# Kernel tuning notes

Hardware: AMD Instinct MI355X
Metric: run time of the kernel (lower is better)

The kernel has to match this reference:

```python
import jax, jax.numpy as jnp
import numpy as np

KNN = 4
H = 0.03


def setup_inputs() -> dict:
    key = jax.random.key(0)
    pc = jax.random.normal(key, (8, 4096, 3), dtype=jnp.float32)  # [B, N, 3]
    return {"pc": pc}


def reference(pc) -> jnp.ndarray:
    sq = jnp.sum(pc * pc, axis=-1)  # [B, N]
    # dist[b, i, j] = || pc[b,i] - pc[b,j] ||^2
    dist = sq[:, :, None] + sq[:, None, :] - 2.0 * jnp.einsum("bid,bjd->bij", pc, pc)
    dist = jnp.maximum(dist, 0.0)
    # k nearest neighbors with offset=1 (skip self): take smallest KNN+1, drop the first
    neg_top, _ = jax.lax.top_k(-dist, KNN + 1)  # sorted descending -> distances ascending
    knn_dist = -neg_top[..., 1:]  # [B, N, KNN]
    weight = jnp.exp(-knn_dist / (H * H))
    loss = jnp.sum(-knn_dist * weight)
    return loss
```

## Files before the change

kernel.cpp:

```cpp
#include <hip/hip_runtime.h>
#include <math.h>

#define NPTS   4096
#define NB     8
#define IGRP   128
#define NWAVES 16
#define BLK    (NWAVES * 64)
#define JCHUNK (NPTS / NWAVES)
#define INV_H2 (1.0f / (0.03f * 0.03f))
#define INFD   3.0e38f

__device__ __forceinline__ float med3f(float a, float b, float c) {
#if defined(__has_builtin)
#if __has_builtin(__builtin_amdgcn_fmed3f)
  return __builtin_amdgcn_fmed3f(a, b, c);
#else
  return fminf(c, fmaxf(a, b));
#endif
#else
  return fminf(c, fmaxf(a, b));
#endif
}

template <bool CHECK>
__device__ __forceinline__ void scan_range(
    const float4* __restrict__ sP, int lo, int hi, int i0, int i1,
    float mx0, float my0, float mz0, float sq0,
    float mx1, float my1, float mz1, float sq1,
    float& a0, float& a1, float& a2, float& a3,
    float& b0, float& b1, float& b2, float& b3) {
#pragma unroll 8
  for (int j = lo; j < hi; ++j) {
    float4 q = sP[j];
    float u = fmaf(mz0, q.z, q.w);
    u = fmaf(my0, q.y, u);
    u = fmaf(mx0, q.x, u);
    float d0 = u + sq0;
    float v = fmaf(mz1, q.z, q.w);
    v = fmaf(my1, q.y, v);
    v = fmaf(mx1, q.x, v);
    float d1 = v + sq1;
    if (CHECK) {
      d0 = (j == i0) ? INFD : d0;
      d1 = (j == i1) ? INFD : d1;
    }
    a3 = med3f(a2, d0, a3); a2 = med3f(a1, d0, a2);
    a1 = med3f(a0, d0, a1); a0 = fminf(a0, d0);
    b3 = med3f(b2, d1, b3); b2 = med3f(b1, d1, b2);
    b1 = med3f(b0, d1, b1); b0 = fminf(b0, d1);
  }
}

__device__ __forceinline__ float4 merge4(float4 A, float4 B) {
  float L0 = fminf(A.x, B.w), L1 = fminf(A.y, B.z);
  float L2 = fminf(A.z, B.y), L3 = fminf(A.w, B.x);
  float e0 = fminf(L0, L2), e2 = fmaxf(L0, L2);
  float e1 = fminf(L1, L3), e3 = fmaxf(L1, L3);
  return make_float4(fminf(e0, e1), fmaxf(e0, e1), fminf(e2, e3), fmaxf(e2, e3));
}

__global__ __launch_bounds__(BLK)
void repulsion_kernel(const float* __restrict__ pc, float* __restrict__ out) {
  __shared__ float4 sP[NPTS];
  __shared__ float4 cand[NWAVES * IGRP];

  const int blk  = blockIdx.x;
  const int b    = blk >> 5;
  const int g    = blk & 31;
  const int tid  = threadIdx.x;
  const float4* pcv = (const float4*)(pc + (size_t)b * NPTS * 3);

  {
    int k = tid;
    float4 a = pcv[3 * k + 0];
    float4 c = pcv[3 * k + 1];
    float4 e = pcv[3 * k + 2];
    float x0 = a.x, y0 = a.y, z0 = a.z;
    float x1 = a.w, y1 = c.x, z1 = c.y;
    float x2 = c.z, y2 = c.w, z2 = e.x;
    float x3 = e.y, y3 = e.z, z3 = e.w;
    sP[4 * k + 0] = make_float4(x0, y0, z0, fmaf(x0, x0, fmaf(y0, y0, z0 * z0)));
    sP[4 * k + 1] = make_float4(x1, y1, z1, fmaf(x1, x1, fmaf(y1, y1, z1 * z1)));
    sP[4 * k + 2] = make_float4(x2, y2, z2, fmaf(x2, x2, fmaf(y2, y2, z2 * z2)));
    sP[4 * k + 3] = make_float4(x3, y3, z3, fmaf(x3, x3, fmaf(y3, y3, z3 * z3)));
  }
  __syncthreads();

  const int w    = tid >> 6;
  const int lane = tid & 63;
  const int i0   = g * IGRP + lane;
  const int i1   = i0 + 64;

  float4 p0 = sP[i0];
  float4 p1 = sP[i1];
  const float mx0 = -2.0f * p0.x, my0 = -2.0f * p0.y, mz0 = -2.0f * p0.z, sq0 = p0.w;
  const float mx1 = -2.0f * p1.x, my1 = -2.0f * p1.y, mz1 = -2.0f * p1.z, sq1 = p1.w;

  float a0 = INFD, a1 = INFD, a2 = INFD, a3 = INFD;
  float b0 = INFD, b1 = INFD, b2 = INFD, b3 = INFD;

  const int j0 = w * JCHUNK;
  const int selfwave = g >> 1;
  if (w == selfwave) {
    const int s0 = g * IGRP;
    scan_range<false>(sP, j0, s0, i0, i1, mx0, my0, mz0, sq0, mx1, my1, mz1, sq1,
                      a0, a1, a2, a3, b0, b1, b2, b3);
    scan_range<true >(sP, s0, s0 + IGRP, i0, i1, mx0, my0, mz0, sq0, mx1, my1, mz1, sq1,
                      a0, a1, a2, a3, b0, b1, b2, b3);
    scan_range<false>(sP, s0 + IGRP, j0 + JCHUNK, i0, i1, mx0, my0, mz0, sq0, mx1, my1, mz1, sq1,
                      a0, a1, a2, a3, b0, b1, b2, b3);
  } else {
    scan_range<false>(sP, j0, j0 + JCHUNK, i0, i1, mx0, my0, mz0, sq0, mx1, my1, mz1, sq1,
                      a0, a1, a2, a3, b0, b1, b2, b3);
  }

  cand[w * IGRP + lane]      = make_float4(a0, a1, a2, a3);
  cand[w * IGRP + 64 + lane] = make_float4(b0, b1, b2, b3);
  __syncthreads();

  if (tid < IGRP) {
    float4 L[NWAVES];
#pragma unroll
    for (int ww = 0; ww < NWAVES; ++ww) L[ww] = cand[ww * IGRP + tid];
#pragma unroll
    for (int ww = 0; ww < 8; ++ww) L[ww] = merge4(L[2 * ww], L[2 * ww + 1]);
#pragma unroll
    for (int ww = 0; ww < 4; ++ww) L[ww] = merge4(L[2 * ww], L[2 * ww + 1]);
    float4 U = merge4(L[0], L[1]);
    float4 V = merge4(L[2], L[3]);
    float m0 = fminf(U.x, V.w);
    float m1 = fminf(U.y, V.z);
    float m2 = fminf(U.z, V.y);
    float m3 = fminf(U.w, V.x);

    float s = 0.0f;
    s -= m0 * expf(-m0 * INV_H2);
    s -= m1 * expf(-m1 * INV_H2);
    s -= m2 * expf(-m2 * INV_H2);
    s -= m3 * expf(-m3 * INV_H2);

    for (int off = 32; off > 0; off >>= 1) s += __shfl_down(s, off);
    if ((tid & 63) == 0) atomicAdd(out, s);
  }
}

extern "C" void kernel_launch(void* const* d_in, const int* in_sizes, int n_in,
                              void* d_out, int out_size, void* d_ws, size_t ws_size,
                              hipStream_t stream) {
  const float* pc = (const float*)d_in[0];
  float* out = (float*)d_out;
  hipMemsetAsync(out, 0, sizeof(float), stream);
  repulsion_kernel<<<dim3(NB * (NPTS / IGRP)), dim3(BLK), 0, stream>>>(pc, out);
}
```

Before: 85.23 us.

## Split j-range across blocks, 4 queries per thread, merge in second kernel

Raises register blocking so each thread keeps top-4 lists for four query points, cutting LDS loads per distance evaluation. The j range is split across four blocks per query group to keep the grid size up, and partial top-4 lists go to workspace. A second kernel merges them and adds the query's squared norm once, instead of once per candidate. The cost is an extra launch, a round trip of partial lists through global memory, and higher register pressure.

```diff
diff --git a/kernel.cpp b/kernel.cpp
--- a/kernel.cpp
+++ b/kernel.cpp
@@ -3,10 +3,13 @@
 
 #define NPTS   4096
 #define NB     8
-#define IGRP   128
-#define NWAVES 16
+#define IT     4
+#define IGRP   (64 * IT)
+#define JSPLIT 4
+#define JBLK   (NPTS / JSPLIT)
+#define NWAVES 8
 #define BLK    (NWAVES * 64)
-#define JCHUNK (NPTS / NWAVES)
+#define JCHUNK (JBLK / NWAVES)
 #define INV_H2 (1.0f / (0.03f * 0.03f))
 #define INFD   3.0e38f
 
@@ -22,35 +25,6 @@
 #endif
 }
 
-template <bool CHECK>
-__device__ __forceinline__ void scan_range(
-    const float4* __restrict__ sP, int lo, int hi, int i0, int i1,
-    float mx0, float my0, float mz0, float sq0,
-    float mx1, float my1, float mz1, float sq1,
-    float& a0, float& a1, float& a2, float& a3,
-    float& b0, float& b1, float& b2, float& b3) {
-#pragma unroll 8
-  for (int j = lo; j < hi; ++j) {
-    float4 q = sP[j];
-    float u = fmaf(mz0, q.z, q.w);
-    u = fmaf(my0, q.y, u);
-    u = fmaf(mx0, q.x, u);
-    float d0 = u + sq0;
-    float v = fmaf(mz1, q.z, q.w);
-    v = fmaf(my1, q.y, v);
-    v = fmaf(mx1, q.x, v);
-    float d1 = v + sq1;
-    if (CHECK) {
-      d0 = (j == i0) ? INFD : d0;
-      d1 = (j == i1) ? INFD : d1;
-    }
-    a3 = med3f(a2, d0, a3); a2 = med3f(a1, d0, a2);
-    a1 = med3f(a0, d0, a1); a0 = fminf(a0, d0);
-    b3 = med3f(b2, d1, b3); b2 = med3f(b1, d1, b2);
-    b1 = med3f(b0, d1, b1); b0 = fminf(b0, d1);
-  }
-}
-
 __device__ __forceinline__ float4 merge4(float4 A, float4 B) {
   float L0 = fminf(A.x, B.w), L1 = fminf(A.y, B.z);
   float L2 = fminf(A.z, B.y), L3 = fminf(A.w, B.x);
@@ -59,63 +33,88 @@
   return make_float4(fminf(e0, e1), fmaxf(e0, e1), fminf(e2, e3), fmaxf(e2, e3));
 }
 
+template <bool CHECK>
+__device__ __forceinline__ void scan_range(const float4* __restrict__ sP,
+                                           int lo, int hi, const int* __restrict__ ls,
+                                           const float* __restrict__ mx,
+                                           const float* __restrict__ my,
+                                           const float* __restrict__ mz,
+                                           float t[IT][4]) {
+#pragma unroll 4
+  for (int j = lo; j < hi; ++j) {
+    float4 q = sP[j];
+#pragma unroll
+    for (int s = 0; s < IT; ++s) {
+      float u = fmaf(mz[s], q.z, q.w);
+      u = fmaf(my[s], q.y, u);
+      u = fmaf(mx[s], q.x, u);
+      if (CHECK) u = (j == ls[s]) ? INFD : u;
+      t[s][3] = med3f(t[s][2], u, t[s][3]);
+      t[s][2] = med3f(t[s][1], u, t[s][2]);
+      t[s][1] = med3f(t[s][0], u, t[s][1]);
+      t[s][0] = fminf(t[s][0], u);
+    }
+  }
+}
+
 __global__ __launch_bounds__(BLK)
-void repulsion_kernel(const float* __restrict__ pc, float* __restrict__ out) {
-  __shared__ float4 sP[NPTS];
-  __shared__ float4 cand[NWAVES * IGRP];
+void repulsion_k1(const float* __restrict__ pc, float4* __restrict__ ws) {
+  __shared__ float4 buf[2 * JBLK];
+  float4* sP = buf;
 
-  const int blk  = blockIdx.x;
-  const int b    = blk >> 5;
-  const int g    = blk & 31;
-  const int tid  = threadIdx.x;
-  const float4* pcv = (const float4*)(pc + (size_t)b * NPTS * 3);
+  const int blk = blockIdx.x;
+  const int b   = blk >> 6;
+  const int g   = (blk >> 2) & 15;
+  const int js  = blk & 3;
+  const int tid = threadIdx.x;
+  const float* base = pc + (size_t)b * NPTS * 3;
 
-  {
-    int k = tid;
-    float4 a = pcv[3 * k + 0];
-    float4 c = pcv[3 * k + 1];
-    float4 e = pcv[3 * k + 2];
+  if (tid < JBLK / 4) {
+    const float4* pcv = (const float4*)base + (size_t)js * (JBLK * 3 / 4);
+    float4 a = pcv[3 * tid + 0];
+    float4 c = pcv[3 * tid + 1];
+    float4 e = pcv[3 * tid + 2];
     float x0 = a.x, y0 = a.y, z0 = a.z;
     float x1 = a.w, y1 = c.x, z1 = c.y;
     float x2 = c.z, y2 = c.w, z2 = e.x;
     float x3 = e.y, y3 = e.z, z3 = e.w;
-    sP[4 * k + 0] = make_float4(x0, y0, z0, fmaf(x0, x0, fmaf(y0, y0, z0 * z0)));
-    sP[4 * k + 1] = make_float4(x1, y1, z1, fmaf(x1, x1, fmaf(y1, y1, z1 * z1)));
-    sP[4 * k + 2] = make_float4(x2, y2, z2, fmaf(x2, x2, fmaf(y2, y2, z2 * z2)));
-    sP[4 * k + 3] = make_float4(x3, y3, z3, fmaf(x3, x3, fmaf(y3, y3, z3 * z3)));
+    sP[4 * tid + 0] = make_float4(x0, y0, z0, fmaf(x0, x0, fmaf(y0, y0, z0 * z0)));
+    sP[4 * tid + 1] = make_float4(x1, y1, z1, fmaf(x1, x1, fmaf(y1, y1, z1 * z1)));
+    sP[4 * tid + 2] = make_float4(x2, y2, z2, fmaf(x2, x2, fmaf(y2, y2, z2 * z2)));
+    sP[4 * tid + 3] = make_float4(x3, y3, z3, fmaf(x3, x3, fmaf(y3, y3, z3 * z3)));
   }
-  __syncthreads();
 
   const int w    = tid >> 6;
   const int lane = tid & 63;
-  const int i0   = g * IGRP + lane;
-  const int i1   = i0 + 64;
 
-  float4 p0 = sP[i0];
-  float4 p1 = sP[i1];
-  const float mx0 = -2.0f * p0.x, my0 = -2.0f * p0.y, mz0 = -2.0f * p0.z, sq0 = p0.w;
-  const float mx1 = -2.0f * p1.x, my1 = -2.0f * p1.y, mz1 = -2.0f * p1.z, sq1 = p1.w;
-
-  float a0 = INFD, a1 = INFD, a2 = INFD, a3 = INFD;
-  float b0 = INFD, b1 = INFD, b2 = INFD, b3 = INFD;
-
-  const int j0 = w * JCHUNK;
-  const int selfwave = g >> 1;
-  if (w == selfwave) {
-    const int s0 = g * IGRP;
-    scan_range<false>(sP, j0, s0, i0, i1, mx0, my0, mz0, sq0, mx1, my1, mz1, sq1,
-                      a0, a1, a2, a3, b0, b1, b2, b3);
-    scan_range<true >(sP, s0, s0 + IGRP, i0, i1, mx0, my0, mz0, sq0, mx1, my1, mz1, sq1,
-                      a0, a1, a2, a3, b0, b1, b2, b3);
-    scan_range<false>(sP, s0 + IGRP, j0 + JCHUNK, i0, i1, mx0, my0, mz0, sq0, mx1, my1, mz1, sq1,
-                      a0, a1, a2, a3, b0, b1, b2, b3);
-  } else {
-    scan_range<false>(sP, j0, j0 + JCHUNK, i0, i1, mx0, my0, mz0, sq0, mx1, my1, mz1, sq1,
-                      a0, a1, a2, a3, b0, b1, b2, b3);
+  float mx[IT], my[IT], mz[IT];
+  int ls[IT];
+#pragma unroll
+  for (int s = 0; s < IT; ++s) {
+    int gi = g * IGRP + lane + 64 * s;
+    float x = base[3 * gi + 0];
+    float y = base[3 * gi + 1];
+    float z = base[3 * gi + 2];
+    mx[s] = -2.0f * x; my[s] = -2.0f * y; mz[s] = -2.0f * z;
+    ls[s] = gi - js * JBLK;
   }
 
-  cand[w * IGRP + lane]      = make_float4(a0, a1, a2, a3);
-  cand[w * IGRP + 64 + lane] = make_float4(b0, b1, b2, b3);
+  float t[IT][4];
+#pragma unroll
+  for (int s = 0; s < IT; ++s) { t[s][0] = INFD; t[s][1] = INFD; t[s][2] = INFD; t[s][3] = INFD; }
+
+  __syncthreads();
+
+  const int lo = w * JCHUNK, hi = lo + JCHUNK;
+  const bool chk = (js == (g >> 2)) && ((w >> 1) == (g & 3));
+  if (chk) scan_range<true >(sP, lo, hi, ls, mx, my, mz, t);
+  else     scan_range<false>(sP, lo, hi, ls, mx, my, mz, t);
+
+  __syncthreads();
+  float4* cand = buf;
+#pragma unroll
+  for (int s = 0; s < IT; ++s)
+    cand[w * IGRP + lane + 64 * s] = make_float4(t[s][0], t[s][1], t[s][2], t[s][3]);
   __syncthreads();
 
   if (tid < IGRP) {
@@ -123,25 +122,40 @@
 #pragma unroll
     for (int ww = 0; ww < NWAVES; ++ww) L[ww] = cand[ww * IGRP + tid];
 #pragma unroll
-    for (int ww = 0; ww < 8; ++ww) L[ww] = merge4(L[2 * ww], L[2 * ww + 1]);
-#pragma unroll
     for (int ww = 0; ww < 4; ++ww) L[ww] = merge4(L[2 * ww], L[2 * ww + 1]);
-    float4 U = merge4(L[0], L[1]);
-    float4 V = merge4(L[2], L[3]);
-    float m0 = fminf(U.x, V.w);
-    float m1 = fminf(U.y, V.z);
-    float m2 = fminf(U.z, V.y);
-    float m3 = fminf(U.w, V.x);
+    L[0] = merge4(L[0], L[1]);
+    L[1] = merge4(L[2], L[3]);
+    float4 R = merge4(L[0], L[1]);
+    int gi = b * NPTS + g * IGRP + tid;
+    ws[(size_t)gi * JSPLIT + js] = R;
+  }
+}
 
-    float s = 0.0f;
-    s -= m0 * expf(-m0 * INV_H2);
-    s -= m1 * expf(-m1 * INV_H2);
-    s -= m2 * expf(-m2 * INV_H2);
-    s -= m3 * expf(-m3 * INV_H2);
+__global__ __launch_bounds__(256)
+void repulsion_k2(const float* __restrict__ pc, const float4* __restrict__ ws,
+                  float* __restrict__ out) {
+  const int t = blockIdx.x * 256 + threadIdx.x;
+  const float4* w4 = ws + (size_t)t * JSPLIT;
+  float4 L0 = w4[0], L1 = w4[1], L2 = w4[2], L3 = w4[3];
+  float4 A = merge4(L0, L1);
+  float4 Bv = merge4(L2, L3);
+  float f0 = fminf(A.x, Bv.w);
+  float f1 = fminf(A.y, Bv.z);
+  float f2 = fminf(A.z, Bv.y);
+  float f3 = fminf(A.w, Bv.x);
 
-    for (int off = 32; off > 0; off >>= 1) s += __shfl_down(s, off);
-    if ((tid & 63) == 0) atomicAdd(out, s);
-  }
+  float x = pc[3 * t + 0], y = pc[3 * t + 1], z = pc[3 * t + 2];
+  float sqi = fmaf(x, x, fmaf(y, y, z * z));
+
+  float s = 0.0f;
+  float m;
+  m = fmaxf(f0 + sqi, 0.0f); s -= m * expf(-m * INV_H2);
+  m = fmaxf(f1 + sqi, 0.0f); s -= m * expf(-m * INV_H2);
+  m = fmaxf(f2 + sqi, 0.0f); s -= m * expf(-m * INV_H2);
+  m = fmaxf(f3 + sqi, 0.0f); s -= m * expf(-m * INV_H2);
+
+  for (int off = 32; off > 0; off >>= 1) s += __shfl_down(s, off);
+  if ((threadIdx.x & 63) == 0) atomicAdd(out, s);
 }
 
 extern "C" void kernel_launch(void* const* d_in, const int* in_sizes, int n_in,
@@ -149,6 +163,8 @@
                               hipStream_t stream) {
   const float* pc = (const float*)d_in[0];
   float* out = (float*)d_out;
+  float4* ws = (float4*)d_ws;
   hipMemsetAsync(out, 0, sizeof(float), stream);
-  repulsion_kernel<<<dim3(NB * (NPTS / IGRP)), dim3(BLK), 0, stream>>>(pc, out);
+  repulsion_k1<<<dim3(NB * 16 * JSPLIT), dim3(BLK), 0, stream>>>(pc, ws);
+  repulsion_k2<<<dim3(NB * NPTS / 256), dim3(256), 0, stream>>>(pc, ws, out);
 }
```

Result: slower. 90.06 us (+5.7%).

## Split into three kernels and skip top-k updates for distant candidates

Applied to the files above, without the earlier changes.

Precomputing the augmented points (coordinates plus squared norm) now happens in a separate kernel that writes them to workspace. The main kernel streams j-points from global memory at a uniform address. Each thread inserts a candidate into its top-4 network only when the partial distance is below a cutoff, so most of the med3 insertion work is skipped. A third kernel merges the 16 per-chunk top-4 lists, adds the squared norm back, clamps, and reduces. This adds launch and global-memory traffic and relies on the loss contribution beyond the cutoff being negligible, which holds because the exponential weight is tiny there.

```diff
diff --git a/kernel.cpp b/kernel.cpp
--- a/kernel.cpp
+++ b/kernel.cpp
@@ -3,10 +3,14 @@
 
 #define NPTS   4096
 #define NB     8
-#define IGRP   128
-#define NWAVES 16
-#define BLK    (NWAVES * 64)
-#define JCHUNK (NPTS / NWAVES)
+#define NPTOT  (NB * NPTS)
+#define IT     2
+#define BLKT   512
+#define IBLK   (BLKT * IT)
+#define NIG    (NPTOT / IBLK)
+#define NJC    16
+#define JBLK   (NPTS / NJC)
+#define THETA  0.025f
 #define INV_H2 (1.0f / (0.03f * 0.03f))
 #define INFD   3.0e38f
 
@@ -22,35 +26,6 @@
 #endif
 }
 
-template <bool CHECK>
-__device__ __forceinline__ void scan_range(
-    const float4* __restrict__ sP, int lo, int hi, int i0, int i1,
-    float mx0, float my0, float mz0, float sq0,
-    float mx1, float my1, float mz1, float sq1,
-    float& a0, float& a1, float& a2, float& a3,
-    float& b0, float& b1, float& b2, float& b3) {
-#pragma unroll 8
-  for (int j = lo; j < hi; ++j) {
-    float4 q = sP[j];
-    float u = fmaf(mz0, q.z, q.w);
-    u = fmaf(my0, q.y, u);
-    u = fmaf(mx0, q.x, u);
-    float d0 = u + sq0;
-    float v = fmaf(mz1, q.z, q.w);
-    v = fmaf(my1, q.y, v);
-    v = fmaf(mx1, q.x, v);
-    float d1 = v + sq1;
-    if (CHECK) {
-      d0 = (j == i0) ? INFD : d0;
-      d1 = (j == i1) ? INFD : d1;
-    }
-    a3 = med3f(a2, d0, a3); a2 = med3f(a1, d0, a2);
-    a1 = med3f(a0, d0, a1); a0 = fminf(a0, d0);
-    b3 = med3f(b2, d1, b3); b2 = med3f(b1, d1, b2);
-    b1 = med3f(b0, d1, b1); b0 = fminf(b0, d1);
-  }
-}
-
 __device__ __forceinline__ float4 merge4(float4 A, float4 B) {
   float L0 = fminf(A.x, B.w), L1 = fminf(A.y, B.z);
   float L2 = fminf(A.z, B.y), L3 = fminf(A.w, B.x);
@@ -59,89 +34,110 @@
   return make_float4(fminf(e0, e1), fmaxf(e0, e1), fminf(e2, e3), fmaxf(e2, e3));
 }
 
-__global__ __launch_bounds__(BLK)
-void repulsion_kernel(const float* __restrict__ pc, float* __restrict__ out) {
-  __shared__ float4 sP[NPTS];
-  __shared__ float4 cand[NWAVES * IGRP];
+__global__ __launch_bounds__(256)
+void repulsion_k0(const float* __restrict__ pc, float4* __restrict__ qarr) {
+  const int k = blockIdx.x * 256 + threadIdx.x;
+  const float4* pcv = (const float4*)pc;
+  float4 a = pcv[3 * k + 0];
+  float4 c = pcv[3 * k + 1];
+  float4 e = pcv[3 * k + 2];
+  float x0 = a.x, y0 = a.y, z0 = a.z;
+  float x1 = a.w, y1 = c.x, z1 = c.y;
+  float x2 = c.z, y2 = c.w, z2 = e.x;
+  float x3 = e.y, y3 = e.z, z3 = e.w;
+  qarr[4 * k + 0] = make_float4(x0, y0, z0, fmaf(x0, x0, fmaf(y0, y0, z0 * z0)));
+  qarr[4 * k + 1] = make_float4(x1, y1, z1, fmaf(x1, x1, fmaf(y1, y1, z1 * z1)));
+  qarr[4 * k + 2] = make_float4(x2, y2, z2, fmaf(x2, x2, fmaf(y2, y2, z2 * z2)));
+  qarr[4 * k + 3] = make_float4(x3, y3, z3, fmaf(x3, x3, fmaf(y3, y3, z3 * z3)));
+}
 
-  const int blk  = blockIdx.x;
-  const int b    = blk >> 5;
-  const int g    = blk & 31;
-  const int tid  = threadIdx.x;
-  const float4* pcv = (const float4*)(pc + (size_t)b * NPTS * 3);
+__global__ __launch_bounds__(BLKT)
+void repulsion_k1(const float4* __restrict__ qarr, float4* __restrict__ ws) {
+  const int blk = blockIdx.x;
+  const int ig  = blk >> 4;
+  const int jc  = blk & 15;
+  const int b   = ig >> 2;
+  const int tid = threadIdx.x;
 
-  {
-    int k = tid;
-    float4 a = pcv[3 * k + 0];
-    float4 c = pcv[3 * k + 1];
-    float4 e = pcv[3 * k + 2];
-    float x0 = a.x, y0 = a.y, z0 = a.z;
-    float x1 = a.w, y1 = c.x, z1 = c.y;
-    float x2 = c.z, y2 = c.w, z2 = e.x;
-    float x3 = e.y, y3 = e.z, z3 = e.w;
-    sP[4 * k + 0] = make_float4(x0, y0, z0, fmaf(x0, x0, fmaf(y0, y0, z0 * z0)));
-    sP[4 * k + 1] = make_float4(x1, y1, z1, fmaf(x1, x1, fmaf(y1, y1, z1 * z1)));
-    sP[4 * k + 2] = make_float4(x2, y2, z2, fmaf(x2, x2, fmaf(y2, y2, z2 * z2)));
-    sP[4 * k + 3] = make_float4(x3, y3, z3, fmaf(x3, x3, fmaf(y3, y3, z3 * z3)));
-  }
-  __syncthreads();
+  const int gi0 = ig * IBLK + tid;
+  const int gi1 = gi0 + BLKT;
+  float4 p0 = qarr[gi0];
+  float4 p1 = qarr[gi1];
+  const float mx0 = -2.0f * p0.x, my0 = -2.0f * p0.y, mz0 = -2.0f * p0.z;
+  const float mx1 = -2.0f * p1.x, my1 = -2.0f * p1.y, mz1 = -2.0f * p1.z;
+  const float c0 = THETA - p0.w;
+  const float c1 = THETA - p1.w;
 
-  const int w    = tid >> 6;
-  const int lane = tid & 63;
-  const int i0   = g * IGRP + lane;
-  const int i1   = i0 + 64;
+  const int jg0 = b * NPTS + jc * JBLK;
+  const float4* __restrict__ qj = qarr + jg0;
 
-  float4 p0 = sP[i0];
-  float4 p1 = sP[i1];
-  const float mx0 = -2.0f * p0.x, my0 = -2.0f * p0.y, mz0 = -2.0f * p0.z, sq0 = p0.w;
-  const float mx1 = -2.0f * p1.x, my1 = -2.0f * p1.y, mz1 = -2.0f * p1.z, sq1 = p1.w;
+  float r0 = INFD, r1 = INFD, r2 = INFD, r3 = INFD;
+  float s0 = INFD, s1 = INFD, s2 = INFD, s3 = INFD;
 
-  float a0 = INFD, a1 = INFD, a2 = INFD, a3 = INFD;
-  float b0 = INFD, b1 = INFD, b2 = INFD, b3 = INFD;
+  auto body = [&](float4 q, int jg) {
+    float u0 = fmaf(mx0, q.x, fmaf(my0, q.y, fmaf(mz0, q.z, q.w)));
+    float u1 = fmaf(mx1, q.x, fmaf(my1, q.y, fmaf(mz1, q.z, q.w)));
+    if (u0 < c0) {
+      float v0 = (jg == gi0) ? INFD : u0;
+      r3 = med3f(r2, v0, r3); r2 = med3f(r1, v0, r2);
+      r1 = med3f(r0, v0, r1); r0 = fminf(r0, v0);
+    }
+    if (u1 < c1) {
+      float v1 = (jg == gi1) ? INFD : u1;
+      s3 = med3f(s2, v1, s3); s2 = med3f(s1, v1, s2);
+      s1 = med3f(s0, v1, s1); s0 = fminf(s0, v1);
+    }
+  };
 
-  const int j0 = w * JCHUNK;
-  const int selfwave = g >> 1;
-  if (w == selfwave) {
-    const int s0 = g * IGRP;
-    scan_range<false>(sP, j0, s0, i0, i1, mx0, my0, mz0, sq0, mx1, my1, mz1, sq1,
-                      a0, a1, a2, a3, b0, b1, b2, b3);
-    scan_range<true >(sP, s0, s0 + IGRP, i0, i1, mx0, my0, mz0, sq0, mx1, my1, mz1, sq1,
-                      a0, a1, a2, a3, b0, b1, b2, b3);
-    scan_range<false>(sP, s0 + IGRP, j0 + JCHUNK, i0, i1, mx0, my0, mz0, sq0, mx1, my1, mz1, sq1,
-                      a0, a1, a2, a3, b0, b1, b2, b3);
-  } else {
-    scan_range<false>(sP, j0, j0 + JCHUNK, i0, i1, mx0, my0, mz0, sq0, mx1, my1, mz1, sq1,
-                      a0, a1, a2, a3, b0, b1, b2, b3);
+  for (int j = 0; j < JBLK; j += 8) {
+    float4 q0 = qj[j + 0];
+    float4 q1 = qj[j + 1];
+    float4 q2 = qj[j + 2];
+    float4 q3 = qj[j + 3];
+    float4 q4 = qj[j + 4];
+    float4 q5 = qj[j + 5];
+    float4 q6 = qj[j + 6];
+    float4 q7 = qj[j + 7];
+    body(q0, jg0 + j + 0);
+    body(q1, jg0 + j + 1);
+    body(q2, jg0 + j + 2);
+    body(q3, jg0 + j + 3);
+    body(q4, jg0 + j + 4);
+    body(q5, jg0 + j + 5);
+    body(q6, jg0 + j + 6);
+    body(q7, jg0 + j + 7);
   }
 
-  cand[w * IGRP + lane]      = make_float4(a0, a1, a2, a3);
-  cand[w * IGRP + 64 + lane] = make_float4(b0, b1, b2, b3);
-  __syncthreads();
+  ws[(size_t)gi0 * NJC + jc] = make_float4(r0, r1, r2, r3);
+  ws[(size_t)gi1 * NJC + jc] = make_float4(s0, s1, s2, s3);
+}
 
-  if (tid < IGRP) {
-    float4 L[NWAVES];
+__global__ __launch_bounds__(256)
+void repulsion_k2(const float4* __restrict__ qarr, const float4* __restrict__ ws,
+                  float* __restrict__ out) {
+  const int t = blockIdx.x * 256 + threadIdx.x;
+  const float4* w4 = ws + (size_t)t * NJC;
+  float4 L[NJC];
 #pragma unroll
-    for (int ww = 0; ww < NWAVES; ++ww) L[ww] = cand[ww * IGRP + tid];
+  for (int k = 0; k < NJC; ++k) L[k] = w4[k];
 #pragma unroll
-    for (int ww = 0; ww < 8; ++ww) L[ww] = merge4(L[2 * ww], L[2 * ww + 1]);
+  for (int k = 0; k < 8; ++k) L[k] = merge4(L[2 * k], L[2 * k + 1]);
 #pragma unroll
-    for (int ww = 0; ww < 4; ++ww) L[ww] = merge4(L[2 * ww], L[2 * ww + 1]);
-    float4 U = merge4(L[0], L[1]);
-    float4 V = merge4(L[2], L[3]);
-    float m0 = fminf(U.x, V.w);
-    float m1 = fminf(U.y, V.z);
-    float m2 = fminf(U.z, V.y);
-    float m3 = fminf(U.w, V.x);
+  for (int k = 0; k < 4; ++k) L[k] = merge4(L[2 * k], L[2 * k + 1]);
+  L[0] = merge4(L[0], L[1]);
+  L[1] = merge4(L[2], L[3]);
+  float4 F = merge4(L[0], L[1]);
 
-    float s = 0.0f;
-    s -= m0 * expf(-m0 * INV_H2);
-    s -= m1 * expf(-m1 * INV_H2);
-    s -= m2 * expf(-m2 * INV_H2);
-    s -= m3 * expf(-m3 * INV_H2);
+  const float sqi = qarr[t].w;
+  float su = 0.0f;
+  float m;
+  m = fminf(fmaxf(F.x + sqi, 0.0f), 0.5f); su -= m * expf(-m * INV_H2);
+  m = fminf(fmaxf(F.y + sqi, 0.0f), 0.5f); su -= m * expf(-m * INV_H2);
+  m = fminf(fmaxf(F.z + sqi, 0.0f), 0.5f); su -= m * expf(-m * INV_H2);
+  m = fminf(fmaxf(F.w + sqi, 0.0f), 0.5f); su -= m * expf(-m * INV_H2);
 
-    for (int off = 32; off > 0; off >>= 1) s += __shfl_down(s, off);
-    if ((tid & 63) == 0) atomicAdd(out, s);
-  }
+  for (int off = 32; off > 0; off >>= 1) su += __shfl_down(su, off);
+  if ((threadIdx.x & 63) == 0) atomicAdd(out, su);
 }
 
 extern "C" void kernel_launch(void* const* d_in, const int* in_sizes, int n_in,
@@ -149,6 +145,10 @@
                               hipStream_t stream) {
   const float* pc = (const float*)d_in[0];
   float* out = (float*)d_out;
+  float4* qarr = (float4*)d_ws;
+  float4* ws   = qarr + NPTOT;
   hipMemsetAsync(out, 0, sizeof(float), stream);
-  repulsion_kernel<<<dim3(NB * (NPTS / IGRP)), dim3(BLK), 0, stream>>>(pc, out);
+  repulsion_k0<<<dim3(NPTOT / 4 / 256), dim3(256), 0, stream>>>(pc, qarr);
+  repulsion_k1<<<dim3(NIG * NJC), dim3(BLKT), 0, stream>>>(qarr, ws);
+  repulsion_k2<<<dim3(NPTOT / 256), dim3(256), 0, stream>>>(qarr, ws, out);
 }
```

After: 94.56 us. +10.9%, slower.
